# Kernel tuning notes

Hardware: AMD Instinct MI355X
Metric: run time of the kernel (lower is better)

Reference implementation:

```python
import jax, jax.numpy as jnp
import numpy as np

EPS = 1e-7  # keras backend.epsilon()
NUM_ROUTING = 3


def squash(v, axis=-1):
    s2 = jnp.sum(jnp.square(v), axis=axis, keepdims=True)
    scale = s2 / (1.0 + s2) / jnp.sqrt(s2 + EPS)
    return scale * v


def setup_inputs() -> dict:
    key = jax.random.key(0)
    k1, k2 = jax.random.split(key)
    B, I, Q = 64, 2048, 16      # batch, input_num_capsule, input_dim_capsule
    J, P = 32, 32               # num_capsule, dim_capsule
    inputs = jax.random.normal(k1, (B, I, Q), dtype=jnp.float32)
    # glorot-ish scale for W: [num_capsule, input_num_capsule, dim_capsule, input_dim_capsule]
    W = jax.random.normal(k2, (J, I, P, Q), dtype=jnp.float32) * (1.0 / np.sqrt(Q))
    return {"inputs": inputs, "W": W}


def reference(inputs, W):
    # inputs_hat[b,j,i,p] = sum_q inputs[b,i,q] * W[j,i,p,q]
    hat = jnp.einsum('biq,jipq->bjip', inputs, W)
    hat_stop = jax.lax.stop_gradient(hat)
    B, J, I, P = hat.shape
    b = jnp.zeros((B, J, I), dtype=hat.dtype)
    for _ in range(NUM_ROUTING - 1):
        c = jax.nn.softmax(b, axis=1)                       # softmax over num_capsule axis
        v = squash(jnp.einsum('bji,bjip->bjp', c, hat_stop))
        b = b + jnp.einsum('bjp,bjip->bji', v, hat_stop)
    c = jax.nn.softmax(b, axis=1)
    return squash(jnp.einsum('bji,bjip->bjp', c, hat))      # [B, J, P]
```

## Files before the change

kernel.cpp:

```cpp
#include <hip/hip_runtime.h>

typedef _Float16 h8 __attribute__((ext_vector_type(8)));
typedef _Float16 h4 __attribute__((ext_vector_type(4)));
typedef float f4 __attribute__((ext_vector_type(4)));

constexpr int NB = 64;
constexpr int NI = 2048;
constexpr int NQ = 16;
constexpr int NJ = 32;
constexpr int NP = 32;
constexpr int NIP = NI / 2;
constexpr int VSZ = NB * NJ * NP;
constexpr int ZBLK = 16;


__global__ __launch_bounds__(256)
void xpack_kernel(const float* __restrict__ X, h8* __restrict__ xp,
                  f4* __restrict__ zbase)
{
    const int bid = blockIdx.x;
    const int t = threadIdx.x;
    if (bid >= NIP) {
        const f4 z = {0.f, 0.f, 0.f, 0.f};
        const int base = (bid - NIP) * 256 + t;
#pragma unroll
        for (int k = 0; k < 12; ++k) zbase[base + k * 4096] = z;
        return;
    }
    const int ip = bid;
    const int bf = t >> 6, l = t & 63;
    const int b = (l & 15) + 16 * bf;
    const int i = 2 * ip + (l >= 32 ? 1 : 0);
    const int q0 = ((l >> 4) & 1) * 8;
    const float* xs = X + ((size_t)b * NI + i) * NQ + q0;
    const float4 u = *reinterpret_cast<const float4*>(xs);
    const float4 v = *reinterpret_cast<const float4*>(xs + 4);
    h8 h;
    h[0] = (_Float16)u.x; h[1] = (_Float16)u.y; h[2] = (_Float16)u.z; h[3] = (_Float16)u.w;
    h[4] = (_Float16)v.x; h[5] = (_Float16)v.y; h[6] = (_Float16)v.z; h[7] = (_Float16)v.w;
    xp[(size_t)(ip * 4 + bf) * 64 + l] = h;
}

__device__ inline float sqscale(float s2)
{
    return s2 / ((1.f + s2) * sqrtf(s2 + 1e-7f));
}

__global__ __launch_bounds__(512)
void wacc_kernel(const float* __restrict__ Wg, const h8* __restrict__ xp,
                 h8* __restrict__ wp, float* __restrict__ ACC)
{
    const int t = threadIdx.x, wv = t >> 6, l = t & 63;
    const int j = blockIdx.x >> 4, is = blockIdx.x & 15;
    const int ioff = (l >= 32) ? 1 : 0;
    const int q0 = ((l >> 4) & 1) * 8;
    const int pbase = is * 64 + wv * 8;

    f4 D[2][4];
#pragma unroll
    for (int pf = 0; pf < 2; ++pf)
#pragma unroll
        for (int bf = 0; bf < 4; ++bf) { f4 Z = {0.f, 0.f, 0.f, 0.f}; D[pf][bf] = Z; }

    const float* wgl = Wg + ((size_t)j * NI + ioff) * (NP * NQ) + (size_t)(l & 15) * NQ + q0;

    f4 u0, u1, v0, v1;
    {
        const float* s0 = wgl + (size_t)(2 * pbase) * (NP * NQ);
        u0 = *reinterpret_cast<const f4*>(s0);
        u1 = *reinterpret_cast<const f4*>(s0 + 4);
        v0 = *reinterpret_cast<const f4*>(s0 + 16 * NQ);
        v1 = *reinterpret_cast<const f4*>(s0 + 16 * NQ + 4);
    }

#pragma unroll 1
    for (int ipl = 0; ipl < 8; ++ipl) {
        const int ipg = pbase + ipl;
        const int nip = (ipl < 7) ? ipg + 1 : ipg;
        f4 nu0, nu1, nv0, nv1;
        {
            const float* s0 = wgl + (size_t)(2 * nip) * (NP * NQ);
            nu0 = *reinterpret_cast<const f4*>(s0);
            nu1 = *reinterpret_cast<const f4*>(s0 + 4);
            nv0 = *reinterpret_cast<const f4*>(s0 + 16 * NQ);
            nv1 = *reinterpret_cast<const f4*>(s0 + 16 * NQ + 4);
        }
        const h8* xpb = xp + (size_t)ipg * 4 * 64 + l;
        const h8 B0 = xpb[0], B1 = xpb[64], B2 = xpb[128], B3 = xpb[192];

        h8 A0, A1;
#pragma unroll
        for (int e = 0; e < 4; ++e) {
            A0[e] = (_Float16)u0[e]; A0[e + 4] = (_Float16)u1[e];
            A1[e] = (_Float16)v0[e]; A1[e + 4] = (_Float16)v1[e];
        }
        const size_t wo = ((size_t)j * NIP + ipg) * 2 * 64 + l;
        wp[wo] = A0;
        wp[wo + 64] = A1;
        D[0][0] = __builtin_amdgcn_mfma_f32_16x16x32_f16(A0, B0, D[0][0], 0, 0, 0);
        D[1][0] = __builtin_amdgcn_mfma_f32_16x16x32_f16(A1, B0, D[1][0], 0, 0, 0);
        D[0][1] = __builtin_amdgcn_mfma_f32_16x16x32_f16(A0, B1, D[0][1], 0, 0, 0);
        D[1][1] = __builtin_amdgcn_mfma_f32_16x16x32_f16(A1, B1, D[1][1], 0, 0, 0);
        D[0][2] = __builtin_amdgcn_mfma_f32_16x16x32_f16(A0, B2, D[0][2], 0, 0, 0);
        D[1][2] = __builtin_amdgcn_mfma_f32_16x16x32_f16(A1, B2, D[1][2], 0, 0, 0);
        D[0][3] = __builtin_amdgcn_mfma_f32_16x16x32_f16(A0, B3, D[0][3], 0, 0, 0);
        D[1][3] = __builtin_amdgcn_mfma_f32_16x16x32_f16(A1, B3, D[1][3], 0, 0, 0);
        u0 = nu0; u1 = nu1; v0 = nv0; v1 = nv1;
    }

    __shared__ float R[8][64 * 36];
#pragma unroll
    for (int pf = 0; pf < 2; ++pf)
#pragma unroll
        for (int bf = 0; bf < 4; ++bf) {
            const int b = (l & 15) + 16 * bf, p = (l >> 4) * 4 + 16 * pf;
            *reinterpret_cast<f4*>(&R[wv][b * 36 + p]) = D[pf][bf];
        }
    __syncthreads();
#pragma unroll
    for (int k = 0; k < 4; ++k) {
        const int id = t + k * 512;
        const int b = id >> 5, p = id & 31;
        float s = 0.f;
#pragma unroll
        for (int w8 = 0; w8 < 8; ++w8) s += R[w8][b * 36 + p];
        atomicAdd(ACC + ((size_t)b * NJ + j) * NP + p, s);
    }
}

template <int SMODE>
__global__ __launch_bounds__(512)
void logits_kernel(const h8* __restrict__ wp, const h8* __restrict__ xp,
                   const float* __restrict__ U1, const float* __restrict__ U2,
                   _Float16* __restrict__ cp)
{
    __shared__ float L[8][32][64];
    const int t = threadIdx.x, wv = t >> 6, l = t & 63;
    const int i0 = blockIdx.x * 8;
    const int ip0 = blockIdx.x * 4;
    const bool lo = l >= 32;
    h8 zh;
#pragma unroll
    for (int e = 0; e < 8; ++e) zh[e] = (_Float16)0.f;

#pragma unroll 1
    for (int jj = 0; jj < 4; ++jj) {
        const int j = wv * 4 + jj;

        float sreg[4][8];
#pragma unroll
        for (int bf = 0; bf < 4; ++bf) {
            const int b = (l & 15) + 16 * bf;
            const size_t base = ((size_t)b * NJ + j) * NP + (l >> 4) * 4;
            float va[8];
#pragma unroll
            for (int pf = 0; pf < 2; ++pf) {
                const f4 u = *reinterpret_cast<const f4*>(U1 + base + 16 * pf);
#pragma unroll
                for (int r = 0; r < 4; ++r) va[pf * 4 + r] = u[r] * (1.f / 32.f);
            }
            float s2 = 0.f;
#pragma unroll
            for (int e = 0; e < 8; ++e) s2 += va[e] * va[e];
            s2 += __shfl_xor(s2, 16);
            s2 += __shfl_xor(s2, 32);
            const float sc1 = sqscale(s2);
#pragma unroll
            for (int e = 0; e < 8; ++e) sreg[bf][e] = va[e] * sc1;

            if (SMODE == 1) {
                float vb[8];
#pragma unroll
                for (int pf = 0; pf < 2; ++pf) {
                    const f4 u = *reinterpret_cast<const f4*>(U2 + base + 16 * pf);
#pragma unroll
                    for (int r = 0; r < 4; ++r) vb[pf * 4 + r] = u[r];
                }
                float t2 = 0.f;
#pragma unroll
                for (int e = 0; e < 8; ++e) t2 += vb[e] * vb[e];
                t2 += __shfl_xor(t2, 16);
                t2 += __shfl_xor(t2, 32);
                const float sc2 = sqscale(t2);
#pragma unroll
                for (int e = 0; e < 8; ++e) sreg[bf][e] += vb[e] * sc2;
            }
        }

        const h8* wj = wp + (size_t)j * NIP * 2 * 64 + l;
        h8 A0 = wj[(size_t)ip0 * 128];
        h8 A1 = wj[(size_t)ip0 * 128 + 64];

#pragma unroll 1
        for (int ipl = 0; ipl < 4; ++ipl) {
            const int ipg = ip0 + ipl;
            const int nip = (ipl < 3) ? ipg + 1 : ipg;
            h8 nA0 = wj[(size_t)nip * 128];
            h8 nA1 = wj[(size_t)nip * 128 + 64];

            const h8* xpb = xp + (size_t)ipg * 4 * 64 + l;

#pragma unroll
            for (int half = 0; half < 2; ++half) {
                f4 D[2][4];
#pragma unroll
                for (int pf = 0; pf < 2; ++pf)
#pragma unroll
                    for (int bf = 0; bf < 4; ++bf) { f4 Z = {0.f, 0.f, 0.f, 0.f}; D[pf][bf] = Z; }
#pragma unroll
                for (int bfp = 0; bfp < 2; ++bfp) {
                    const h8 Ba = xpb[(2 * bfp) * 64];
                    const h8 Bb = xpb[(2 * bfp + 1) * 64];
                    const h8 Bma = ((half == 0) == lo) ? zh : Ba;
                    const h8 Bmb = ((half == 0) == lo) ? zh : Bb;
                    D[0][2 * bfp]     = __builtin_amdgcn_mfma_f32_16x16x32_f16(A0, Bma, D[0][2 * bfp], 0, 0, 0);
                    D[1][2 * bfp]     = __builtin_amdgcn_mfma_f32_16x16x32_f16(A1, Bma, D[1][2 * bfp], 0, 0, 0);
                    D[0][2 * bfp + 1] = __builtin_amdgcn_mfma_f32_16x16x32_f16(A0, Bmb, D[0][2 * bfp + 1], 0, 0, 0);
                    D[1][2 * bfp + 1] = __builtin_amdgcn_mfma_f32_16x16x32_f16(A1, Bmb, D[1][2 * bfp + 1], 0, 0, 0);
                }
                float part[4];
#pragma unroll
                for (int bf = 0; bf < 4; ++bf) {
                    float p_ = 0.f;
#pragma unroll
                    for (int pf = 0; pf < 2; ++pf)
#pragma unroll
                        for (int r = 0; r < 4; ++r) p_ += sreg[bf][pf * 4 + r] * D[pf][bf][r];
                    p_ += __shfl_xor(p_, 16);
                    p_ += __shfl_xor(p_, 32);
                    part[bf] = p_;
                }
                const int hb = l >> 4;
                const float wval = hb == 0 ? part[0] : hb == 1 ? part[1] : hb == 2 ? part[2] : part[3];
                L[ipl * 2 + half][j][(l & 15) + 16 * hb] = wval;
            }
            A0 = nA0; A1 = nA1;
        }
    }
    __syncthreads();

    {
        const int b = t & 63, ii = t >> 6;
        float lv[32];
        float m = -1e30f;
#pragma unroll
        for (int j = 0; j < 32; ++j) { lv[j] = L[ii][j][b]; m = fmaxf(m, lv[j]); }
        float s = 0.f;
#pragma unroll
        for (int j = 0; j < 32; ++j) { lv[j] = __expf(lv[j] - m); s += lv[j]; }
        const float inv = 1.f / s;
#pragma unroll
        for (int j = 0; j < 32; ++j) L[ii][j][b] = lv[j] * inv;
    }
    __syncthreads();

    {
        const int jw = t >> 4, r = t & 15;
#pragma unroll 1
        for (int ii = 0; ii < 8; ++ii) {
            h4 c4;
#pragma unroll
            for (int e = 0; e < 4; ++e) c4[e] = (_Float16)L[ii][jw][16 * e + r];
            *reinterpret_cast<h4*>(cp + ((size_t)jw * NI + i0 + ii) * 64 + r * 4) = c4;
        }
    }
}

__global__ __launch_bounds__(512)
void accum_kernel(const h8* __restrict__ wp, const h8* __restrict__ xp,
                  const _Float16* __restrict__ cp, float* __restrict__ ACC)
{
    const int t = threadIdx.x, wv = t >> 6, l = t & 63;
    const int j = blockIdx.x >> 4, is = blockIdx.x & 15;
    const int ioff = (l >= 32) ? 1 : 0;

    f4 D[2][4];
#pragma unroll
    for (int pf = 0; pf < 2; ++pf)
#pragma unroll
        for (int bf = 0; bf < 4; ++bf) { f4 Z = {0.f, 0.f, 0.f, 0.f}; D[pf][bf] = Z; }

    const int pbase = is * 64 + wv * 8;
    const h8* wj = wp + (size_t)j * NIP * 2 * 64 + l;
    const _Float16* cj = cp + ((size_t)j * NI + ioff) * 64 + (l & 15) * 4;

    h8 A0 = wj[(size_t)pbase * 128];
    h8 A1 = wj[(size_t)pbase * 128 + 64];

#pragma unroll 1
    for (int ipl = 0; ipl < 8; ++ipl) {
        const int ipg = pbase + ipl;
        const int nip = (ipl < 7) ? ipg + 1 : ipg;
        h8 nA0 = wj[(size_t)nip * 128];
        h8 nA1 = wj[(size_t)nip * 128 + 64];

        const h8* xpb = xp + (size_t)ipg * 4 * 64 + l;
        const h4 c4 = *reinterpret_cast<const h4*>(cj + (size_t)(2 * ipg) * 64);
        const h8 b0 = xpb[0] * c4[0];
        const h8 b1 = xpb[64] * c4[1];
        const h8 b2 = xpb[128] * c4[2];
        const h8 b3 = xpb[192] * c4[3];

        D[0][0] = __builtin_amdgcn_mfma_f32_16x16x32_f16(A0, b0, D[0][0], 0, 0, 0);
        D[1][0] = __builtin_amdgcn_mfma_f32_16x16x32_f16(A1, b0, D[1][0], 0, 0, 0);
        D[0][1] = __builtin_amdgcn_mfma_f32_16x16x32_f16(A0, b1, D[0][1], 0, 0, 0);
        D[1][1] = __builtin_amdgcn_mfma_f32_16x16x32_f16(A1, b1, D[1][1], 0, 0, 0);
        D[0][2] = __builtin_amdgcn_mfma_f32_16x16x32_f16(A0, b2, D[0][2], 0, 0, 0);
        D[1][2] = __builtin_amdgcn_mfma_f32_16x16x32_f16(A1, b2, D[1][2], 0, 0, 0);
        D[0][3] = __builtin_amdgcn_mfma_f32_16x16x32_f16(A0, b3, D[0][3], 0, 0, 0);
        D[1][3] = __builtin_amdgcn_mfma_f32_16x16x32_f16(A1, b3, D[1][3], 0, 0, 0);
        A0 = nA0; A1 = nA1;
    }

    __shared__ float R[8][64 * 36];
#pragma unroll
    for (int pf = 0; pf < 2; ++pf)
#pragma unroll
        for (int bf = 0; bf < 4; ++bf) {
            const int b = (l & 15) + 16 * bf, p = (l >> 4) * 4 + 16 * pf;
            *reinterpret_cast<f4*>(&R[wv][b * 36 + p]) = D[pf][bf];
        }
    __syncthreads();
#pragma unroll
    for (int k = 0; k < 4; ++k) {
        const int id = t + k * 512;
        const int b = id >> 5, p = id & 31;
        float s = 0.f;
#pragma unroll
        for (int w8 = 0; w8 < 8; ++w8) s += R[w8][b * 36 + p];
        atomicAdd(ACC + ((size_t)b * NJ + j) * NP + p, s);
    }
}

__global__ __launch_bounds__(256)
void squash_kernel(const float* __restrict__ U, float* __restrict__ OUT)
{
    const int t   = threadIdx.x;
    const int row = blockIdx.x * 8 + (t >> 5);
    const int p   = t & 31;
    const float val = U[row * 32 + p];
    float sq = val * val;
#pragma unroll
    for (int d = 1; d < 32; d <<= 1) sq += __shfl_xor(sq, d);
    OUT[row * 32 + p] = val * sqscale(sq);
}

extern "C" void kernel_launch(void* const* d_in, const int* in_sizes, int n_in,
                              void* d_out, int out_size, void* d_ws, size_t ws_size,
                              hipStream_t stream)
{
    const float* X  = (const float*)d_in[0];
    const float* Wg = (const float*)d_in[1];
    float* out = (float*)d_out;

    float* v1u = (float*)d_ws;
    float* v2u = v1u + VSZ;
    float* ou  = v2u + VSZ;
    h8* xp = (h8*)((char*)d_ws + (size_t)3 * VSZ * 4);
    _Float16* cp = (_Float16*)((char*)xp + (size_t)NIP * 4 * 64 * 16);
    h8* wpk = (h8*)((char*)cp + (size_t)NJ * NI * 64 * 2);

    xpack_kernel<<<NIP + ZBLK, 256, 0, stream>>>(X, xp, (f4*)d_ws);

    wacc_kernel<<<512, 512, 0, stream>>>(Wg, xp, wpk, v1u);

    logits_kernel<0><<<NI / 8, 512, 0, stream>>>(wpk, xp, v1u, nullptr, cp);
    accum_kernel<<<512, 512, 0, stream>>>(wpk, xp, cp, v2u);

    logits_kernel<1><<<NI / 8, 512, 0, stream>>>(wpk, xp, v1u, v2u, cp);
    accum_kernel<<<512, 512, 0, stream>>>(wpk, xp, cp, ou);

    squash_kernel<<<VSZ / 256, 256, 0, stream>>>(ou, out);
}
```

Baseline: 143.2 us.

## Precompute squashed routing vectors, halve logits blocks, add setprio and deeper prefetch

Result: slower. 189.9 us (+32.6%).

```diff
diff --git a/kernel.cpp b/kernel.cpp
--- a/kernel.cpp
+++ b/kernel.cpp
@@ -97,6 +97,7 @@
         const size_t wo = ((size_t)j * NIP + ipg) * 2 * 64 + l;
         wp[wo] = A0;
         wp[wo + 64] = A1;
+        __builtin_amdgcn_s_setprio(1);
         D[0][0] = __builtin_amdgcn_mfma_f32_16x16x32_f16(A0, B0, D[0][0], 0, 0, 0);
         D[1][0] = __builtin_amdgcn_mfma_f32_16x16x32_f16(A1, B0, D[1][0], 0, 0, 0);
         D[0][1] = __builtin_amdgcn_mfma_f32_16x16x32_f16(A0, B1, D[0][1], 0, 0, 0);
@@ -105,6 +106,7 @@
         D[1][2] = __builtin_amdgcn_mfma_f32_16x16x32_f16(A1, B2, D[1][2], 0, 0, 0);
         D[0][3] = __builtin_amdgcn_mfma_f32_16x16x32_f16(A0, B3, D[0][3], 0, 0, 0);
         D[1][3] = __builtin_amdgcn_mfma_f32_16x16x32_f16(A1, B3, D[1][3], 0, 0, 0);
+        __builtin_amdgcn_s_setprio(0);
         u0 = nu0; u1 = nu1; v0 = nv0; v1 = nv1;
     }
 
@@ -124,20 +126,18 @@
         float s = 0.f;
 #pragma unroll
         for (int w8 = 0; w8 < 8; ++w8) s += R[w8][b * 36 + p];
-        atomicAdd(ACC + ((size_t)b * NJ + j) * NP + p, s);
-    }
-}
-
-template <int SMODE>
-__global__ __launch_bounds__(512)
+        atomicAdd(ACC + ((size_t)b * NJ + j) * NP + p, s * (1.f / 32.f));
+    }
+}
+
+__global__ __launch_bounds__(512, 4)
 void logits_kernel(const h8* __restrict__ wp, const h8* __restrict__ xp,
-                   const float* __restrict__ U1, const float* __restrict__ U2,
-                   _Float16* __restrict__ cp)
-{
-    __shared__ float L[8][32][64];
+                   const float* __restrict__ S, _Float16* __restrict__ cp)
+{
+    __shared__ float L[4][32][64];
     const int t = threadIdx.x, wv = t >> 6, l = t & 63;
-    const int i0 = blockIdx.x * 8;
-    const int ip0 = blockIdx.x * 4;
+    const int i0 = blockIdx.x * 4;
+    const int ip0 = blockIdx.x * 2;
     const bool lo = l >= 32;
     h8 zh;
 #pragma unroll
@@ -152,61 +152,30 @@
         for (int bf = 0; bf < 4; ++bf) {
             const int b = (l & 15) + 16 * bf;
             const size_t base = ((size_t)b * NJ + j) * NP + (l >> 4) * 4;
-            float va[8];
-#pragma unroll
-            for (int pf = 0; pf < 2; ++pf) {
-                const f4 u = *reinterpret_cast<const f4*>(U1 + base + 16 * pf);
-#pragma unroll
-                for (int r = 0; r < 4; ++r) va[pf * 4 + r] = u[r] * (1.f / 32.f);
-            }
-            float s2 = 0.f;
-#pragma unroll
-            for (int e = 0; e < 8; ++e) s2 += va[e] * va[e];
-            s2 += __shfl_xor(s2, 16);
-            s2 += __shfl_xor(s2, 32);
-            const float sc1 = sqscale(s2);
-#pragma unroll
-            for (int e = 0; e < 8; ++e) sreg[bf][e] = va[e] * sc1;
-
-            if (SMODE == 1) {
-                float vb[8];
-#pragma unroll
-                for (int pf = 0; pf < 2; ++pf) {
-                    const f4 u = *reinterpret_cast<const f4*>(U2 + base + 16 * pf);
-#pragma unroll
-                    for (int r = 0; r < 4; ++r) vb[pf * 4 + r] = u[r];
-                }
-                float t2 = 0.f;
-#pragma unroll
-                for (int e = 0; e < 8; ++e) t2 += vb[e] * vb[e];
-                t2 += __shfl_xor(t2, 16);
-                t2 += __shfl_xor(t2, 32);
-                const float sc2 = sqscale(t2);
-#pragma unroll
-                for (int e = 0; e < 8; ++e) sreg[bf][e] += vb[e] * sc2;
-            }
+            const f4 u0 = *reinterpret_cast<const f4*>(S + base);
+            const f4 u1 = *reinterpret_cast<const f4*>(S + base + 16);
+#pragma unroll
+            for (int r = 0; r < 4; ++r) { sreg[bf][r] = u0[r]; sreg[bf][4 + r] = u1[r]; }
         }
 
         const h8* wj = wp + (size_t)j * NIP * 2 * 64 + l;
-        h8 A0 = wj[(size_t)ip0 * 128];
-        h8 A1 = wj[(size_t)ip0 * 128 + 64];
-
-#pragma unroll 1
-        for (int ipl = 0; ipl < 4; ++ipl) {
-            const int ipg = ip0 + ipl;
-            const int nip = (ipl < 3) ? ipg + 1 : ipg;
-            h8 nA0 = wj[(size_t)nip * 128];
-            h8 nA1 = wj[(size_t)nip * 128 + 64];
-
-            const h8* xpb = xp + (size_t)ipg * 4 * 64 + l;
+
+        f4 D[2][4];
+#pragma unroll
+        for (int pf = 0; pf < 2; ++pf)
+#pragma unroll
+            for (int bf = 0; bf < 4; ++bf) { f4 Z = {0.f, 0.f, 0.f, 0.f}; D[pf][bf] = Z; }
+        float prev[4] = {0.f, 0.f, 0.f, 0.f};
+
+#pragma unroll
+        for (int ipl = 0; ipl < 2; ++ipl) {
+            const h8 A0 = wj[(size_t)(ip0 + ipl) * 128];
+            const h8 A1 = wj[(size_t)(ip0 + ipl) * 128 + 64];
+            const h8* xpb = xp + (size_t)(ip0 + ipl) * 4 * 64 + l;
 
 #pragma unroll
             for (int half = 0; half < 2; ++half) {
-                f4 D[2][4];
-#pragma unroll
-                for (int pf = 0; pf < 2; ++pf)
-#pragma unroll
-                    for (int bf = 0; bf < 4; ++bf) { f4 Z = {0.f, 0.f, 0.f, 0.f}; D[pf][bf] = Z; }
+                __builtin_amdgcn_s_setprio(1);
 #pragma unroll
                 for (int bfp = 0; bfp < 2; ++bfp) {
                     const h8 Ba = xpb[(2 * bfp) * 64];
@@ -218,28 +187,30 @@
                     D[0][2 * bfp + 1] = __builtin_amdgcn_mfma_f32_16x16x32_f16(A0, Bmb, D[0][2 * bfp + 1], 0, 0, 0);
                     D[1][2 * bfp + 1] = __builtin_amdgcn_mfma_f32_16x16x32_f16(A1, Bmb, D[1][2 * bfp + 1], 0, 0, 0);
                 }
+                __builtin_amdgcn_s_setprio(0);
                 float part[4];
 #pragma unroll
                 for (int bf = 0; bf < 4; ++bf) {
-                    float p_ = 0.f;
+                    float cur = 0.f;
 #pragma unroll
                     for (int pf = 0; pf < 2; ++pf)
 #pragma unroll
-                        for (int r = 0; r < 4; ++r) p_ += sreg[bf][pf * 4 + r] * D[pf][bf][r];
-                    p_ += __shfl_xor(p_, 16);
-                    p_ += __shfl_xor(p_, 32);
-                    part[bf] = p_;
+                        for (int r = 0; r < 4; ++r) cur += sreg[bf][pf * 4 + r] * D[pf][bf][r];
+                    float dd = cur - prev[bf];
+                    prev[bf] = cur;
+                    dd += __shfl_xor(dd, 16);
+                    dd += __shfl_xor(dd, 32);
+                    part[bf] = dd;
                 }
                 const int hb = l >> 4;
                 const float wval = hb == 0 ? part[0] : hb == 1 ? part[1] : hb == 2 ? part[2] : part[3];
                 L[ipl * 2 + half][j][(l & 15) + 16 * hb] = wval;
             }
-            A0 = nA0; A1 = nA1;
         }
     }
     __syncthreads();
 
-    {
+    if (t < 256) {
         const int b = t & 63, ii = t >> 6;
         float lv[32];
         float m = -1e30f;
@@ -256,8 +227,8 @@
 
     {
         const int jw = t >> 4, r = t & 15;
-#pragma unroll 1
-        for (int ii = 0; ii < 8; ++ii) {
+#pragma unroll
+        for (int ii = 0; ii < 4; ++ii) {
             h4 c4;
 #pragma unroll
             for (int e = 0; e < 4; ++e) c4[e] = (_Float16)L[ii][jw][16 * e + r];
@@ -266,7 +237,7 @@
     }
 }
 
-__global__ __launch_bounds__(512)
+__global__ __launch_bounds__(512, 4)
 void accum_kernel(const h8* __restrict__ wp, const h8* __restrict__ xp,
                   const _Float16* __restrict__ cp, float* __restrict__ ACC)
 {
@@ -284,15 +255,17 @@
     const h8* wj = wp + (size_t)j * NIP * 2 * 64 + l;
     const _Float16* cj = cp + ((size_t)j * NI + ioff) * 64 + (l & 15) * 4;
 
-    h8 A0 = wj[(size_t)pbase * 128];
-    h8 A1 = wj[(size_t)pbase * 128 + 64];
+    h8 Aa0 = wj[(size_t)pbase * 128];
+    h8 Aa1 = wj[(size_t)pbase * 128 + 64];
+    h8 Ab0 = wj[(size_t)(pbase + 1) * 128];
+    h8 Ab1 = wj[(size_t)(pbase + 1) * 128 + 64];
 
 #pragma unroll 1
     for (int ipl = 0; ipl < 8; ++ipl) {
         const int ipg = pbase + ipl;
-        const int nip = (ipl < 7) ? ipg + 1 : ipg;
-        h8 nA0 = wj[(size_t)nip * 128];
-        h8 nA1 = wj[(size_t)nip * 128 + 64];
+        const int nip = pbase + ((ipl + 2 < 8) ? ipl + 2 : 7);
+        h8 Ac0 = wj[(size_t)nip * 128];
+        h8 Ac1 = wj[(size_t)nip * 128 + 64];
 
         const h8* xpb = xp + (size_t)ipg * 4 * 64 + l;
         const h4 c4 = *reinterpret_cast<const h4*>(cj + (size_t)(2 * ipg) * 64);
@@ -301,15 +274,17 @@
         const h8 b2 = xpb[128] * c4[2];
         const h8 b3 = xpb[192] * c4[3];
 
-        D[0][0] = __builtin_amdgcn_mfma_f32_16x16x32_f16(A0, b0, D[0][0], 0, 0, 0);
-        D[1][0] = __builtin_amdgcn_mfma_f32_16x16x32_f16(A1, b0, D[1][0], 0, 0, 0);
-        D[0][1] = __builtin_amdgcn_mfma_f32_16x16x32_f16(A0, b1, D[0][1], 0, 0, 0);
-        D[1][1] = __builtin_amdgcn_mfma_f32_16x16x32_f16(A1, b1, D[1][1], 0, 0, 0);
-        D[0][2] = __builtin_amdgcn_mfma_f32_16x16x32_f16(A0, b2, D[0][2], 0, 0, 0);
-        D[1][2] = __builtin_amdgcn_mfma_f32_16x16x32_f16(A1, b2, D[1][2], 0, 0, 0);
-        D[0][3] = __builtin_amdgcn_mfma_f32_16x16x32_f16(A0, b3, D[0][3], 0, 0, 0);
-        D[1][3] = __builtin_amdgcn_mfma_f32_16x16x32_f16(A1, b3, D[1][3], 0, 0, 0);
-        A0 = nA0; A1 = nA1;
+        __builtin_amdgcn_s_setprio(1);
+        D[0][0] = __builtin_amdgcn_mfma_f32_16x16x32_f16(Aa0, b0, D[0][0], 0, 0, 0);
+        D[1][0] = __builtin_amdgcn_mfma_f32_16x16x32_f16(Aa1, b0, D[1][0], 0, 0, 0);
+        D[0][1] = __builtin_amdgcn_mfma_f32_16x16x32_f16(Aa0, b1, D[0][1], 0, 0, 0);
+        D[1][1] = __builtin_amdgcn_mfma_f32_16x16x32_f16(Aa1, b1, D[1][1], 0, 0, 0);
+        D[0][2] = __builtin_amdgcn_mfma_f32_16x16x32_f16(Aa0, b2, D[0][2], 0, 0, 0);
+        D[1][2] = __builtin_amdgcn_mfma_f32_16x16x32_f16(Aa1, b2, D[1][2], 0, 0, 0);
+        D[0][3] = __builtin_amdgcn_mfma_f32_16x16x32_f16(Aa0, b3, D[0][3], 0, 0, 0);
+        D[1][3] = __builtin_amdgcn_mfma_f32_16x16x32_f16(Aa1, b3, D[1][3], 0, 0, 0);
+        __builtin_amdgcn_s_setprio(0);
+        Aa0 = Ab0; Aa1 = Ab1; Ab0 = Ac0; Ab1 = Ac1;
     }
 
     __shared__ float R[8][64 * 36];
@@ -333,7 +308,8 @@
 }
 
 __global__ __launch_bounds__(256)
-void squash_kernel(const float* __restrict__ U, float* __restrict__ OUT)
+void squash_kernel(const float* __restrict__ U, const float* __restrict__ ADD,
+                   float* __restrict__ OUT)
 {
     const int t   = threadIdx.x;
     const int row = blockIdx.x * 8 + (t >> 5);
@@ -342,7 +318,9 @@
     float sq = val * val;
 #pragma unroll
     for (int d = 1; d < 32; d <<= 1) sq += __shfl_xor(sq, d);
-    OUT[row * 32 + p] = val * sqscale(sq);
+    float o = val * sqscale(sq);
+    if (ADD != nullptr) o += ADD[row * 32 + p];
+    OUT[row * 32 + p] = o;
 }
 
 extern "C" void kernel_launch(void* const* d_in, const int* in_sizes, int n_in,
@@ -356,7 +334,9 @@
     float* v1u = (float*)d_ws;
     float* v2u = v1u + VSZ;
     float* ou  = v2u + VSZ;
-    h8* xp = (h8*)((char*)d_ws + (size_t)3 * VSZ * 4);
+    float* S2  = ou  + VSZ;
+    float* S3  = S2  + VSZ;
+    h8* xp = (h8*)((char*)d_ws + (size_t)5 * VSZ * 4);
     _Float16* cp = (_Float16*)((char*)xp + (size_t)NIP * 4 * 64 * 16);
     h8* wpk = (h8*)((char*)cp + (size_t)NJ * NI * 64 * 2);
 
@@ -364,11 +344,13 @@
 
     wacc_kernel<<<512, 512, 0, stream>>>(Wg, xp, wpk, v1u);
 
-    logits_kernel<0><<<NI / 8, 512, 0, stream>>>(wpk, xp, v1u, nullptr, cp);
+    squash_kernel<<<VSZ / 256, 256, 0, stream>>>(v1u, nullptr, S2);
+    logits_kernel<<<NI / 4, 512, 0, stream>>>(wpk, xp, S2, cp);
     accum_kernel<<<512, 512, 0, stream>>>(wpk, xp, cp, v2u);
 
-    logits_kernel<1><<<NI / 8, 512, 0, stream>>>(wpk, xp, v1u, v2u, cp);
+    squash_kernel<<<VSZ / 256, 256, 0, stream>>>(v2u, S2, S3);
+    logits_kernel<<<NI / 4, 512, 0, stream>>>(wpk, xp, S3, cp);
     accum_kernel<<<512, 512, 0, stream>>>(wpk, xp, cp, ou);
 
-    squash_kernel<<<VSZ / 256, 256, 0, stream>>>(ou, out);
-}
+    squash_kernel<<<VSZ / 256, 256, 0, stream>>>(ou, nullptr, out);
+}
```
